# Kernel optimization log

Hardware: AMD Instinct MI355X
Metric: run time of the kernel (lower is better)

## Reference

```python
import jax, jax.numpy as jnp
import numpy as np

HEADS = 16
HIDDEN = 1024
D_HEAD = HIDDEN // HEADS
SCALE = float(D_HEAD) ** 0.5


def setup_inputs() -> dict:
    key = jax.random.key(0)
    ks = jax.random.split(key, 11)
    B, L = 2, 2048
    x = jax.random.normal(ks[0], (B, L, HIDDEN), dtype=jnp.float32)
    # 0/1 padding mask, broadcast over heads and query positions
    mask = jax.random.randint(ks[1], (B, 1, 1, L), 0, 2).astype(jnp.float32)
    s = 1.0 / np.sqrt(HIDDEN)
    Wq = jax.random.normal(ks[2], (HIDDEN, HIDDEN), dtype=jnp.float32) * s
    bq = jax.random.normal(ks[3], (HIDDEN,), dtype=jnp.float32) * s
    Wk = jax.random.normal(ks[4], (HIDDEN, HIDDEN), dtype=jnp.float32) * s
    bk = jax.random.normal(ks[5], (HIDDEN,), dtype=jnp.float32) * s
    Wv = jax.random.normal(ks[6], (HIDDEN, HIDDEN), dtype=jnp.float32) * s
    bv = jax.random.normal(ks[7], (HIDDEN,), dtype=jnp.float32) * s
    Wo = jax.random.normal(ks[8], (HIDDEN, HIDDEN), dtype=jnp.float32) * s
    bo = jax.random.normal(ks[9], (HIDDEN,), dtype=jnp.float32) * s
    return {"x": x, "mask": mask, "Wq": Wq, "bq": bq, "Wk": Wk, "bk": bk,
            "Wv": Wv, "bv": bv, "Wo": Wo, "bo": bo}


def reference(x, mask, Wq, bq, Wk, bk, Wv, bv, Wo, bo):
    B, L, _ = x.shape
    # projections (Linear: x @ W + b), split heads -> [B, H, L, Dh]
    def proj(W, b):
        return (jnp.dot(x, W) + b).reshape(B, L, HEADS, D_HEAD).transpose(0, 2, 1, 3)
    q = proj(Wq, bq)
    k = proj(Wk, bk)
    v = proj(Wv, bv)
    # scaled dot-product with additive mask: scores [B, H, Lq, Lk]
    scores = jnp.einsum('bhqd,bhkd->bhqk', q, k) / SCALE + mask * (-10000.0)
    attn = jax.nn.softmax(scores, axis=-1)  # dropout p=0.0 -> identity
    out = jnp.einsum('bhqk,bhkd->bhqd', attn, v)
    out = out.transpose(0, 2, 1, 3).reshape(B, L, HIDDEN)
    return jnp.dot(out, Wo) + bo
```

## Files before the change

### kernel.cpp

```cpp
#include <hip/hip_runtime.h>
#include <math.h>

typedef unsigned short u16;
typedef short v8s __attribute__((ext_vector_type(8)));
typedef float v4f __attribute__((ext_vector_type(4)));
typedef float v16f __attribute__((ext_vector_type(16)));

#define HIDDEN 1024
#define L_SEQ 2048
#define NH 16
#define DH 64
#define NKMAX 1280

#define QSCALE 0.18033688011112042f

__device__ __forceinline__ u16 f2bf(float f) {
  union { float f; unsigned int i; } c; c.f = f;
  unsigned int x = c.i;
  unsigned int r = (x + 0x7fffu + ((x >> 16) & 1u)) >> 16;
  return (u16)r;
}

#if defined(__has_builtin)
#if __has_builtin(__builtin_amdgcn_cvt_pk_bf16_f32)
#define HAS_PKBF 1
#endif
#if __has_builtin(__builtin_amdgcn_exp2f)
#define EXP2(x) __builtin_amdgcn_exp2f(x)
#endif
#if __has_builtin(__builtin_amdgcn_rcpf)
#define RCP(x) __builtin_amdgcn_rcpf(x)
#endif
#endif
#ifndef EXP2
#define EXP2(x) exp2f(x)
#endif
#ifndef RCP
#define RCP(x) (1.0f / (x))
#endif

__device__ __forceinline__ unsigned pkbf(float a, float b) {
#ifdef HAS_PKBF
  typedef __bf16 v2bf __attribute__((ext_vector_type(2)));
  union { v2bf v; unsigned u; } c;
  c.v = __builtin_amdgcn_cvt_pk_bf16_f32(a, b);
  return c.u;
#else
  return (unsigned)f2bf(a) | ((unsigned)f2bf(b) << 16);
#endif
}

__device__ __forceinline__ void gload16(const void* g, void* l) {
  void* gg = const_cast<void*>(g);
  __builtin_amdgcn_global_load_lds(
      (__attribute__((address_space(1))) void*)gg,
      (__attribute__((address_space(3))) void*)l, 16, 0, 0);
}

__device__ __forceinline__ v16f vzero16() {
  v16f z;
#pragma unroll
  for (int i = 0; i < 16; ++i) z[i] = 0.f;
  return z;
}

__global__ __launch_bounds__(256) void prep(
    const float* __restrict__ x, u16* __restrict__ xb,
    const float* __restrict__ Wq, const float* __restrict__ Wk,
    const float* __restrict__ Wv, const float* __restrict__ Wo,
    u16* __restrict__ WtQ, u16* __restrict__ WtK,
    u16* __restrict__ WtV, u16* __restrict__ WtO,
    const float* __restrict__ maskg, u16* __restrict__ keep,
    unsigned* __restrict__ nkslot) {
  const int bid = blockIdx.x;
  const int t = threadIdx.x;

  if (bid < 2048) {
    const int i = (bid * 256 + t) * 8;
    const float4 a = *(const float4*)(x + i);
    const float4 b = *(const float4*)(x + i + 4);
    unsigned o[4] = {pkbf(a.x, a.y), pkbf(a.z, a.w), pkbf(b.x, b.y), pkbf(b.z, b.w)};
    *(uint4*)(xb + i) = *(const uint4*)o;
    return;
  }

  if (bid < 6144) {
    const int m = bid - 2048;
    const int z = m >> 10;
    const int rem = m & 1023;
    const int bx = rem & 31, by = rem >> 5;
    const float* src; u16* dst;
    if (z == 0) { src = Wq; dst = WtQ; }
    else if (z == 1) { src = Wk; dst = WtK; }
    else if (z == 2) { src = Wv; dst = WtV; }
    else { src = Wo; dst = WtO; }

    __shared__ u16 tile[32][33];
    const int tx = t & 31, ty = t >> 5;
    const int xcol = bx * 32 + tx;
    const int y0 = by * 32;
#pragma unroll
    for (int i = ty; i < 32; i += 8)
      tile[i][tx] = f2bf(src[(size_t)(y0 + i) * HIDDEN + xcol]);
    __syncthreads();
    const int xo = y0 + tx;
#pragma unroll
    for (int i = ty; i < 32; i += 8)
      dst[(size_t)(bx * 32 + i) * HIDDEN + xo] = tile[tx][i];
    return;
  }

  if (t < 64) {
    const int b = bid - 6144;
    const int lane = t;
    const float* mp = maskg + b * L_SEQ;
    int cnt = 0;
#pragma unroll 1
    for (int j = 0; j < 32; ++j) cnt += (mp[lane * 32 + j] == 0.0f) ? 1 : 0;
    int inc = cnt;
#pragma unroll
    for (int off = 1; off < 64; off <<= 1) {
      const int v = __shfl_up(inc, off, 64);
      if (lane >= off) inc += v;
    }
    int base = inc - cnt;
    u16* kp = keep + b * L_SEQ;
#pragma unroll 1
    for (int j = 0; j < 32; ++j) {
      const int k = lane * 32 + j;
      if (mp[k] == 0.0f) kp[base++] = (u16)k;
    }
    const int total = __shfl(inc, 63, 64);
    for (int i = total + lane; i < NKMAX; i += 64) kp[i] = 0;
    if (lane == 0) nkslot[b] = (unsigned)total;
  }
}

__global__ __launch_bounds__(256) void gemm128(
    const u16* __restrict__ A,
    const u16* __restrict__ B0, const u16* __restrict__ B1, const u16* __restrict__ B2,
    const float* __restrict__ bias0, const float* __restrict__ bias1, const float* __restrict__ bias2,
    u16* __restrict__ C0, u16* __restrict__ C1, u16* __restrict__ C2,
    float* __restrict__ Cf, const u16* __restrict__ keep,
    const unsigned* __restrict__ nkslot,
    int qkv_mode) {
  __shared__ __align__(16) u16 As[128 * 32];
  __shared__ __align__(16) u16 Bs[128 * 32];

  const u16* Bt; const float* bias; u16* C;
  if (blockIdx.z == 0) { Bt = B0; bias = bias0; C = C0; }
  else if (blockIdx.z == 1) { Bt = B1; bias = bias1; C = C1; }
  else { Bt = B2; bias = bias2; C = C2; }
  const int mode = qkv_mode ? (blockIdx.z == 0 ? 1 : (blockIdx.z == 1 ? 2 : 3)) : 0;
  const float oscale = (mode == 1) ? QSCALE : 1.0f;

  const int t = threadIdx.x;
  const int lane = t & 63;
  const int wave = t >> 6;
  const int quad = lane >> 4;
  const int l16 = lane & 15;
  const int wm = wave >> 1;
  const int wn = wave & 1;

  const int n0 = blockIdx.x * 128;
  const int sr = t >> 2;
  const int sc = (t & 3) * 8;

  int m0 = blockIdx.y * 128;
  int kvb = 0;
  const u16* Ag0;
  const u16* Ag1;
  if (mode == 2 || mode == 3) {
    const int y = blockIdx.y;
    if (y >= 20) return;
    kvb = y / 10;
    m0 = (y % 10) * 128;
    const unsigned nk = nkslot[kvb];
    if ((unsigned)m0 >= ((nk + 63u) & ~63u)) return;
    const int sr0 = keep[kvb * L_SEQ + m0 + sr];
    const int sr1 = keep[kvb * L_SEQ + m0 + 64 + sr];
    Ag0 = A + ((size_t)(kvb * L_SEQ + sr0)) * HIDDEN + sc;
    Ag1 = A + ((size_t)(kvb * L_SEQ + sr1)) * HIDDEN + sc;
  } else {
    Ag0 = A + (size_t)(m0 + sr) * HIDDEN + sc;
    Ag1 = Ag0 + (size_t)64 * HIDDEN;
  }
  const u16* Bg0 = Bt + (size_t)(n0 + sr) * HIDDEN + sc;
  const u16* Bg1 = Bg0 + (size_t)64 * HIDDEN;
  u16* Al0 = &As[sr * 32 + sc];
  u16* Al1 = &As[(64 + sr) * 32 + sc];
  u16* Bl0 = &Bs[sr * 32 + sc];
  u16* Bl1 = &Bs[(64 + sr) * 32 + sc];

  v4f acc[4][4];
#pragma unroll
  for (int mi = 0; mi < 4; ++mi)
#pragma unroll
    for (int ni = 0; ni < 4; ++ni)
      acc[mi][ni] = (v4f){0.f, 0.f, 0.f, 0.f};

  for (int k0 = 0; k0 < HIDDEN; k0 += 32) {
    __syncthreads();
    gload16(Ag0 + k0, Al0);
    gload16(Ag1 + k0, Al1);
    gload16(Bg0 + k0, Bl0);
    gload16(Bg1 + k0, Bl1);
    __syncthreads();

    v8s a[4], b[4];
#pragma unroll
    for (int mi = 0; mi < 4; ++mi)
      a[mi] = *(const v8s*)&As[(wm * 64 + mi * 16 + l16) * 32 + quad * 8];
#pragma unroll
    for (int ni = 0; ni < 4; ++ni)
      b[ni] = *(const v8s*)&Bs[(wn * 64 + ni * 16 + l16) * 32 + quad * 8];
#pragma unroll
    for (int mi = 0; mi < 4; ++mi)
#pragma unroll
      for (int ni = 0; ni < 4; ++ni)
        acc[mi][ni] = __builtin_amdgcn_mfma_f32_16x16x32_bf16(a[mi], b[ni], acc[mi][ni], 0, 0, 0);
  }

#pragma unroll
  for (int ni = 0; ni < 4; ++ni) {
    const int col = n0 + wn * 64 + ni * 16 + l16;
    const float bv = bias[col];
#pragma unroll
    for (int mi = 0; mi < 4; ++mi) {
      const int row0 = m0 + wm * 64 + mi * 16 + quad * 4;
      const float v0 = (acc[mi][ni][0] + bv) * oscale;
      const float v1 = (acc[mi][ni][1] + bv) * oscale;
      const float v2 = (acc[mi][ni][2] + bv) * oscale;
      const float v3 = (acc[mi][ni][3] + bv) * oscale;
      if (mode == 0) {
        Cf[(size_t)(row0 + 0) * HIDDEN + col] = v0;
        Cf[(size_t)(row0 + 1) * HIDDEN + col] = v1;
        Cf[(size_t)(row0 + 2) * HIDDEN + col] = v2;
        Cf[(size_t)(row0 + 3) * HIDDEN + col] = v3;
      } else if (mode == 1) {
        const int hh = col >> 6, d = col & 63;
        const float vv[4] = {v0, v1, v2, v3};
#pragma unroll
        for (int i = 0; i < 4; ++i) {
          const int rr = row0 + i;
          const int bb = rr >> 11, l = rr & 2047;
          C[((size_t)(bb * NH + hh) * L_SEQ + l) * DH + d] = f2bf(vv[i]);
        }
      } else if (mode == 2) {
        const int hh = col >> 6, d = col & 63;
        const float vv[4] = {v0, v1, v2, v3};
#pragma unroll
        for (int i = 0; i < 4; ++i)
          C[((size_t)(kvb * NH + hh) * L_SEQ + row0 + i) * DH + d] = f2bf(vv[i]);
      } else {
        const int hh = col >> 6, d = col & 63;
        unsigned pk[2] = {pkbf(v0, v1), pkbf(v2, v3)};
        *(uint2*)&C[((size_t)((kvb * NH + hh) * DH + d)) * L_SEQ + row0] = *(const uint2*)pk;
      }
    }
  }
}


#define MKPF(dst, P0, P1, P2, P3, P4, P5, P6, P7)                   \
  {                                                                 \
    const unsigned a_ = pkbf(P0, P1), c_ = pkbf(P2, P3);            \
    const unsigned b_ = pkbf(P4, P5), d_ = pkbf(P6, P7);            \
    const unsigned a2_ = (unsigned)__shfl((int)a_, lane ^ 32, 64);  \
    const unsigned b2_ = (unsigned)__shfl((int)b_, lane ^ 32, 64);  \
    const unsigned c2_ = (unsigned)__shfl((int)c_, lane ^ 32, 64);  \
    const unsigned d2_ = (unsigned)__shfl((int)d_, lane ^ 32, 64);  \
    union { unsigned u[4]; v8s v; } f_;                             \
    f_.u[0] = lo32 ? a_ : b2_;                                      \
    f_.u[1] = lo32 ? c_ : d2_;                                      \
    f_.u[2] = lo32 ? a2_ : b_;                                      \
    f_.u[3] = lo32 ? c2_ : d_;                                      \
    dst = f_.v;                                                     \
  }

__global__ __launch_bounds__(256) void attn128(
    const u16* __restrict__ Qg, const u16* __restrict__ Kcg, const u16* __restrict__ VTg,
    const unsigned* __restrict__ nkslot, u16* __restrict__ Og) {
  __shared__ __align__(16) u16 lds[16384];

  const int t = threadIdx.x;
  const int lane = t & 63;
  const int w = t >> 6;
  const int l31 = lane & 31;
  const int hi = lane >> 5;
  const bool lo32 = lane < 32;
  const int e7 = l31 & 7;

  const int q0 = blockIdx.x * 128;
  const int bh = blockIdx.y;
  const int b = bh >> 4;
  const int h = bh & 15;

  const size_t base = (size_t)bh * L_SEQ * DH;
  const u16* Qp = Qg + base;
  const u16* Kp = Kcg + base;
  const u16* VTp = VTg + base;

  const int nkb = (int)nkslot[b];
  const int ntiles = (nkb + 63) >> 6;

  const int r8 = lane >> 3;
  const int sl = lane & 7;
  const int og8 = (sl ^ r8) * 8;
  const int koff = (w * 16 + r8) * DH + og8;
  const int voff = (w * 16 + r8) * L_SEQ + og8;

  gload16(Kp + koff, &lds[(w * 16) * 64]);
  gload16(Kp + koff + 8 * DH, &lds[(w * 16 + 8) * 64]);
  gload16(VTp + voff, &lds[8192 + (w * 16) * 64]);
  gload16(VTp + voff + 8 * L_SEQ, &lds[8192 + (w * 16 + 8) * 64]);

  const int qrow = q0 + w * 32 + l31;
  v8s qf[4];
#pragma unroll
  for (int dc = 0; dc < 4; ++dc)
    qf[dc] = *(const v8s*)&Qp[(size_t)qrow * DH + dc * 16 + hi * 8];

  v16f oacc0 = vzero16(), oacc1 = vzero16();
  float lsum = 0.f;

  for (int n = 0; n < ntiles; ++n) {
    __syncthreads();
    const int ksb = (n & 1) * 4096;
    const int vtb = 8192 + (n & 1) * 4096;
    if (n + 1 < ntiles) {
      const int k1 = (n + 1) * 64;
      const int ksb2 = ((n + 1) & 1) * 4096;
      const int vtb2 = 8192 + ((n + 1) & 1) * 4096;
      gload16(Kp + (size_t)k1 * DH + koff, &lds[ksb2 + (w * 16) * 64]);
      gload16(Kp + (size_t)k1 * DH + koff + 8 * DH, &lds[ksb2 + (w * 16 + 8) * 64]);
      gload16(VTp + voff + k1, &lds[vtb2 + (w * 16) * 64]);
      gload16(VTp + voff + k1 + 8 * L_SEQ, &lds[vtb2 + (w * 16 + 8) * 64]);
    }

    v16f s0 = vzero16(), s1 = vzero16();
#pragma unroll
    for (int dc = 0; dc < 4; ++dc) {
      const int po = ((dc * 2 + hi) ^ e7) * 8;
      const v8s kf0 = *(const v8s*)&lds[ksb + l31 * 64 + po];
      const v8s kf1 = *(const v8s*)&lds[ksb + (32 + l31) * 64 + po];
      s0 = __builtin_amdgcn_mfma_f32_32x32x16_bf16(kf0, qf[dc], s0, 0, 0, 0);
      s1 = __builtin_amdgcn_mfma_f32_32x32x16_bf16(kf1, qf[dc], s1, 0, 0, 0);
    }

    const int kb0 = n * 64;
    float p[32];
#pragma unroll
    for (int r = 0; r < 16; ++r) {
      p[r]      = EXP2(s0[r]);
      p[16 + r] = EXP2(s1[r]);
    }
    if (kb0 + 64 > nkb) {
#pragma unroll
      for (int r = 0; r < 16; ++r) {
        const int kk = kb0 + (r & 3) + 8 * (r >> 2) + 4 * hi;
        if (kk >= nkb) p[r] = 0.f;
        if (kk + 32 >= nkb) p[16 + r] = 0.f;
      }
    }
    {
      float a0 = 0.f, a1 = 0.f, a2 = 0.f, a3 = 0.f;
#pragma unroll
      for (int r = 0; r < 8; ++r) {
        a0 += p[r]; a1 += p[8 + r]; a2 += p[16 + r]; a3 += p[24 + r];
      }
      lsum += (a0 + a1) + (a2 + a3);
    }

    v8s pf0, pf1, pf2, pf3;
    MKPF(pf0, p[0],  p[1],  p[2],  p[3],  p[4],  p[5],  p[6],  p[7]);
    MKPF(pf1, p[8],  p[9],  p[10], p[11], p[12], p[13], p[14], p[15]);
    MKPF(pf2, p[16], p[17], p[18], p[19], p[20], p[21], p[22], p[23]);
    MKPF(pf3, p[24], p[25], p[26], p[27], p[28], p[29], p[30], p[31]);

#pragma unroll
    for (int kc = 0; kc < 4; ++kc) {
      const v8s pb = (kc == 0) ? pf0 : (kc == 1) ? pf1 : (kc == 2) ? pf2 : pf3;
      const int po = ((kc * 2 + hi) ^ e7) * 8;
      const v8s vf0 = *(const v8s*)&lds[vtb + l31 * 64 + po];
      const v8s vf1 = *(const v8s*)&lds[vtb + (32 + l31) * 64 + po];
      oacc0 = __builtin_amdgcn_mfma_f32_32x32x16_bf16(vf0, pb, oacc0, 0, 0, 0);
      oacc1 = __builtin_amdgcn_mfma_f32_32x32x16_bf16(vf1, pb, oacc1, 0, 0, 0);
    }
  }

  const float ltot = lsum + __shfl(lsum, lane ^ 32, 64);
  const float linv = RCP(ltot);

  const size_t ob = ((size_t)(b * L_SEQ + qrow)) * HIDDEN + h * DH;
#pragma unroll
  for (int r = 0; r < 16; r += 2) {
    const int d0 = (r & 3) + 8 * (r >> 2) + 4 * hi;
    const unsigned w0 = pkbf(oacc0[r] * linv, oacc0[r + 1] * linv);
    const unsigned w1 = pkbf(oacc1[r] * linv, oacc1[r + 1] * linv);
    *(unsigned*)&Og[ob + d0] = w0;
    *(unsigned*)&Og[ob + 32 + d0] = w1;
  }
}

extern "C" void kernel_launch(void* const* d_in, const int* in_sizes, int n_in,
                              void* d_out, int out_size, void* d_ws, size_t ws_size,
                              hipStream_t stream) {
  const float* x    = (const float*)d_in[0];
  const float* mask = (const float*)d_in[1];
  const float* Wq   = (const float*)d_in[2];
  const float* bq   = (const float*)d_in[3];
  const float* Wk   = (const float*)d_in[4];
  const float* bk   = (const float*)d_in[5];
  const float* Wv   = (const float*)d_in[6];
  const float* bv   = (const float*)d_in[7];
  const float* Wo   = (const float*)d_in[8];
  const float* bo   = (const float*)d_in[9];
  float* out = (float*)d_out;
  u16* ws = (u16*)d_ws;

  const unsigned M1 = 1u << 20;
  u16* WtQ = ws;
  u16* WtK = ws + M1;
  u16* WtV = ws + 2 * M1;
  u16* WtO = ws + 3 * M1;
  u16* xb  = ws + 4 * M1;
  u16* Qb  = ws + 8 * M1;
  u16* Kc  = ws + 12 * M1;
  u16* VTc = ws + 16 * M1;
  u16* Ob  = ws + 20 * M1;
  u16* keep = ws + 16 * M1 - 8192;
  unsigned* nkslot = (unsigned*)(ws + 16 * M1 - 8192 - 8);

  prep<<<6146, 256, 0, stream>>>(x, xb, Wq, Wk, Wv, Wo, WtQ, WtK, WtV, WtO,
                                 mask, keep, nkslot);
  gemm128<<<dim3(8, 32, 3), 256, 0, stream>>>(xb, WtQ, WtK, WtV, bq, bk, bv,
                                              Qb, Kc, VTc, nullptr, keep, nkslot, 1);
  attn128<<<dim3(16, 32), 256, 0, stream>>>(Qb, Kc, VTc, nkslot, Ob);
  gemm128<<<dim3(8, 32, 1), 256, 0, stream>>>(Ob, WtO, WtO, WtO, bo, bo, bo,
                                              nullptr, nullptr, nullptr, out, nullptr, nullptr, 0);
}
```

Before: 191.7 us.

## Load K and V tiles directly from global into registers, drop LDS staging

The attention kernel no longer stages K and V^T tiles through a double-buffered shared-memory ring with a block-wide barrier each iteration. Instead each wave loads its MFMA operand fragments straight from global memory into registers, prefetching the next tile after the current MFMAs consume the previous one. This removes the per-tile __syncthreads and the LDS write/read traffic. In exchange, each of the four waves in a block now fetches the full K/V tile itself, multiplying global/L2 traffic by four and raising register pressure from the prefetched fragments.

```diff
diff --git a/kernel.cpp b/kernel.cpp
--- a/kernel.cpp
+++ b/kernel.cpp
@@ -281,15 +281,12 @@
 __global__ __launch_bounds__(256) void attn128(
     const u16* __restrict__ Qg, const u16* __restrict__ Kcg, const u16* __restrict__ VTg,
     const unsigned* __restrict__ nkslot, u16* __restrict__ Og) {
-  __shared__ __align__(16) u16 lds[16384];
-
   const int t = threadIdx.x;
   const int lane = t & 63;
   const int w = t >> 6;
   const int l31 = lane & 31;
   const int hi = lane >> 5;
   const bool lo32 = lane < 32;
-  const int e7 = l31 & 7;
 
   const int q0 = blockIdx.x * 128;
   const int bh = blockIdx.y;
@@ -298,67 +295,65 @@
 
   const size_t base = (size_t)bh * L_SEQ * DH;
   const u16* Qp = Qg + base;
-  const u16* Kp = Kcg + base;
-  const u16* VTp = VTg + base;
 
   const int nkb = (int)nkslot[b];
   const int ntiles = (nkb + 63) >> 6;
 
-  const int r8 = lane >> 3;
-  const int sl = lane & 7;
-  const int og8 = (sl ^ r8) * 8;
-  const int koff = (w * 16 + r8) * DH + og8;
-  const int voff = (w * 16 + r8) * L_SEQ + og8;
-
-  gload16(Kp + koff, &lds[(w * 16) * 64]);
-  gload16(Kp + koff + 8 * DH, &lds[(w * 16 + 8) * 64]);
-  gload16(VTp + voff, &lds[8192 + (w * 16) * 64]);
-  gload16(VTp + voff + 8 * L_SEQ, &lds[8192 + (w * 16 + 8) * 64]);
-
   const int qrow = q0 + w * 32 + l31;
   v8s qf[4];
 #pragma unroll
   for (int dc = 0; dc < 4; ++dc)
     qf[dc] = *(const v8s*)&Qp[(size_t)qrow * DH + dc * 16 + hi * 8];
 
+  const u16* kb0 = Kcg + base + (size_t)l31 * DH + hi * 8;
+  const u16* kb1 = Kcg + base + (size_t)(32 + l31) * DH + hi * 8;
+  const u16* vb0 = VTg + base + (size_t)l31 * L_SEQ + hi * 8;
+  const u16* vb1 = VTg + base + (size_t)(32 + l31) * L_SEQ + hi * 8;
+
+  v8s kf[8], vf[8];
+  auto loadK = [&](int n) {
+    const size_t o = (size_t)n * (64 * DH);
+#pragma unroll
+    for (int dc = 0; dc < 4; ++dc) {
+      kf[dc]     = *(const v8s*)(kb0 + o + dc * 16);
+      kf[4 + dc] = *(const v8s*)(kb1 + o + dc * 16);
+    }
+  };
+  auto loadV = [&](int n) {
+    const int o = n * 64;
+#pragma unroll
+    for (int kc = 0; kc < 4; ++kc) {
+      vf[kc]     = *(const v8s*)(vb0 + o + kc * 16);
+      vf[4 + kc] = *(const v8s*)(vb1 + o + kc * 16);
+    }
+  };
+
+  loadK(0);
+  loadV(0);
+
   v16f oacc0 = vzero16(), oacc1 = vzero16();
   float lsum = 0.f;
 
   for (int n = 0; n < ntiles; ++n) {
-    __syncthreads();
-    const int ksb = (n & 1) * 4096;
-    const int vtb = 8192 + (n & 1) * 4096;
-    if (n + 1 < ntiles) {
-      const int k1 = (n + 1) * 64;
-      const int ksb2 = ((n + 1) & 1) * 4096;
-      const int vtb2 = 8192 + ((n + 1) & 1) * 4096;
-      gload16(Kp + (size_t)k1 * DH + koff, &lds[ksb2 + (w * 16) * 64]);
-      gload16(Kp + (size_t)k1 * DH + koff + 8 * DH, &lds[ksb2 + (w * 16 + 8) * 64]);
-      gload16(VTp + voff + k1, &lds[vtb2 + (w * 16) * 64]);
-      gload16(VTp + voff + k1 + 8 * L_SEQ, &lds[vtb2 + (w * 16 + 8) * 64]);
-    }
-
     v16f s0 = vzero16(), s1 = vzero16();
 #pragma unroll
     for (int dc = 0; dc < 4; ++dc) {
-      const int po = ((dc * 2 + hi) ^ e7) * 8;
-      const v8s kf0 = *(const v8s*)&lds[ksb + l31 * 64 + po];
-      const v8s kf1 = *(const v8s*)&lds[ksb + (32 + l31) * 64 + po];
-      s0 = __builtin_amdgcn_mfma_f32_32x32x16_bf16(kf0, qf[dc], s0, 0, 0, 0);
-      s1 = __builtin_amdgcn_mfma_f32_32x32x16_bf16(kf1, qf[dc], s1, 0, 0, 0);
-    }
-
-    const int kb0 = n * 64;
+      s0 = __builtin_amdgcn_mfma_f32_32x32x16_bf16(kf[dc], qf[dc], s0, 0, 0, 0);
+      s1 = __builtin_amdgcn_mfma_f32_32x32x16_bf16(kf[4 + dc], qf[dc], s1, 0, 0, 0);
+    }
+    if (n + 1 < ntiles) loadK(n + 1);
+
+    const int kb_0 = n * 64;
     float p[32];
 #pragma unroll
     for (int r = 0; r < 16; ++r) {
       p[r]      = EXP2(s0[r]);
       p[16 + r] = EXP2(s1[r]);
     }
-    if (kb0 + 64 > nkb) {
+    if (kb_0 + 64 > nkb) {
 #pragma unroll
       for (int r = 0; r < 16; ++r) {
-        const int kk = kb0 + (r & 3) + 8 * (r >> 2) + 4 * hi;
+        const int kk = kb_0 + (r & 3) + 8 * (r >> 2) + 4 * hi;
         if (kk >= nkb) p[r] = 0.f;
         if (kk + 32 >= nkb) p[16 + r] = 0.f;
       }
@@ -381,12 +376,10 @@
 #pragma unroll
     for (int kc = 0; kc < 4; ++kc) {
       const v8s pb = (kc == 0) ? pf0 : (kc == 1) ? pf1 : (kc == 2) ? pf2 : pf3;
-      const int po = ((kc * 2 + hi) ^ e7) * 8;
-      const v8s vf0 = *(const v8s*)&lds[vtb + l31 * 64 + po];
-      const v8s vf1 = *(const v8s*)&lds[vtb + (32 + l31) * 64 + po];
-      oacc0 = __builtin_amdgcn_mfma_f32_32x32x16_bf16(vf0, pb, oacc0, 0, 0, 0);
-      oacc1 = __builtin_amdgcn_mfma_f32_32x32x16_bf16(vf1, pb, oacc1, 0, 0, 0);
-    }
+      oacc0 = __builtin_amdgcn_mfma_f32_32x32x16_bf16(vf[kc], pb, oacc0, 0, 0, 0);
+      oacc1 = __builtin_amdgcn_mfma_f32_32x32x16_bf16(vf[4 + kc], pb, oacc1, 0, 0, 0);
+    }
+    if (n + 1 < ntiles) loadV(n + 1);
   }
 
   const float ltot = lsum + __shfl(lsum, lane ^ 32, 64);
```

New measurement: 221.6 us. 15.6% more time.
